# Optimization experiments

Hardware: AMD Instinct MI355X
Metric: run time of the kernel (lower is better)

Reference implementation:

```python
import jax, jax.numpy as jnp
import numpy as np

B, IMG, TXT = 1, 2048, 256
D_MODEL = 2048
HEADS, HEAD_DIM = 16, 128
INNER = HEADS * HEAD_DIM
EPS = 1e-5
SCALE = HEAD_DIM ** -0.5


def _rmsnorm(x, w):
    # normalize over last dim (head_dim)
    return (x * jax.lax.rsqrt(jnp.mean(x * x, axis=-1, keepdims=True) + EPS)) * w


def _rope(x, cos, sin):
    # x: (B, S, H, D); cos/sin: (S, D) with pairwise-repeated freqs (interleaved convention)
    c = cos[None, :, None, :]
    s = sin[None, :, None, :]
    x1 = x[..., 0::2]
    x2 = x[..., 1::2]
    rot = jnp.stack([-x2, x1], axis=-1).reshape(x.shape)
    return x * c + rot * s


def setup_inputs() -> dict:
    key = jax.random.key(0)
    ks = jax.random.split(key, 12)
    sc_in = D_MODEL ** -0.5
    sc_inner = INNER ** -0.5
    inp = {
        'hidden_states': jax.random.normal(ks[0], (B, IMG, D_MODEL), jnp.float32),
        'encoder_hidden_states': jax.random.normal(ks[1], (B, TXT, D_MODEL), jnp.float32),
    }
    # RoPE tables over the joint (text + image) sequence, interleaved pair layout
    pos = jnp.arange(TXT + IMG, dtype=jnp.float32)
    inv = 1.0 / (10000.0 ** (jnp.arange(0, HEAD_DIM, 2, dtype=jnp.float32) / HEAD_DIM))
    freqs = pos[:, None] * inv[None, :]
    freqs = jnp.repeat(freqs, 2, axis=-1)  # (S, HEAD_DIM)
    inp['freqs_cos'] = jnp.cos(freqs)
    inp['freqs_sin'] = jnp.sin(freqs)
    # parameters (stored (in, out))
    inp['Wqkv'] = jax.random.normal(ks[2], (D_MODEL, 3 * INNER), jnp.float32) * sc_in
    inp['Wqkv_add'] = jax.random.normal(ks[3], (D_MODEL, 3 * INNER), jnp.float32) * sc_in
    inp['b_qkv_add'] = jax.random.normal(ks[4], (3 * INNER,), jnp.float32) * 0.01
    inp['norm_q_w'] = jnp.ones((HEAD_DIM,), jnp.float32)
    inp['norm_k_w'] = jnp.ones((HEAD_DIM,), jnp.float32)
    inp['norm_aq_w'] = jnp.ones((HEAD_DIM,), jnp.float32)
    inp['norm_ak_w'] = jnp.ones((HEAD_DIM,), jnp.float32)
    inp['Wout'] = jax.random.normal(ks[5], (INNER, D_MODEL), jnp.float32) * sc_inner
    inp['b_out'] = jax.random.normal(ks[6], (D_MODEL,), jnp.float32) * 0.01
    inp['Wadd_out'] = jax.random.normal(ks[7], (INNER, D_MODEL), jnp.float32) * sc_inner
    inp['b_add_out'] = jax.random.normal(ks[8], (D_MODEL,), jnp.float32) * 0.01
    return inp


def reference(hidden_states, encoder_hidden_states, freqs_cos, freqs_sin,
              Wqkv, Wqkv_add, b_qkv_add, norm_q_w, norm_k_w, norm_aq_w, norm_ak_w,
              Wout, b_out, Wadd_out, b_add_out):
    b, s_img, _ = hidden_states.shape
    s_txt = encoder_hidden_states.shape[1]

    # fused QKV projection (image stream), chunk q/k/v, unflatten heads
    qkv = hidden_states @ Wqkv  # (B, IMG, 3*INNER)
    q, k, v = jnp.split(qkv, 3, axis=-1)
    q = _rmsnorm(q.reshape(b, s_img, HEADS, HEAD_DIM), norm_q_w)
    k = _rmsnorm(k.reshape(b, s_img, HEADS, HEAD_DIM), norm_k_w)
    v = v.reshape(b, s_img, HEADS, HEAD_DIM)

    # fused QKV projection (text stream, with bias)
    eqkv = encoder_hidden_states @ Wqkv_add + b_qkv_add
    eq, ek, ev = jnp.split(eqkv, 3, axis=-1)
    eq = _rmsnorm(eq.reshape(b, s_txt, HEADS, HEAD_DIM), norm_aq_w)
    ek = _rmsnorm(ek.reshape(b, s_txt, HEADS, HEAD_DIM), norm_ak_w)
    ev = ev.reshape(b, s_txt, HEADS, HEAD_DIM)

    # joint [text; image] concatenation, then RoPE on joint Q/K
    jq = jnp.concatenate([eq, q], axis=1)
    jk = jnp.concatenate([ek, k], axis=1)
    jv = jnp.concatenate([ev, v], axis=1)
    jq = _rope(jq, freqs_cos, freqs_sin)
    jk = _rope(jk, freqs_cos, freqs_sin)

    # non-causal scaled dot-product attention, layout (B, S, H, D)
    scores = jnp.einsum('bqhd,bkhd->bhqk', jq, jk) * SCALE
    probs = jax.nn.softmax(scores, axis=-1)
    out = jnp.einsum('bhqk,bkhd->bqhd', probs, jv)  # (B, S_joint, H, D)
    out = out.reshape(b, s_txt + s_img, INNER)

    enc_out = out[:, :s_txt]
    img_out = out[:, s_txt:]
    img_out = img_out @ Wout + b_out
    enc_out = enc_out @ Wadd_out + b_add_out
    return (img_out, enc_out)
```

## Files before the change

### kernel.cpp

```cpp
#include <hip/hip_runtime.h>
#include <stdint.h>

#define HEADS 16
#define HD 128
#define S_TXT 256
#define S_IMG 2048
#define S_ALL 2304
#define DMODEL 2048
#define N_QKV 6144
#define INNER 2048
#define ATT_EPS 1e-5f
#define ATT_SCALE 0.08838834764831845f
#define LOG2E 1.4426950408889634f
#define MBOUND 16.5f
#define QT_N 18
#define TPS 36

typedef __attribute__((ext_vector_type(8))) __bf16 bf16x8;
typedef __attribute__((ext_vector_type(4))) float f32x4;
typedef __attribute__((ext_vector_type(4))) uint32_t u32x4;

__device__ __forceinline__ uint16_t f2bf(float f) {
  union { float f; uint32_t u; } v; v.f = f;
  uint32_t r = (v.u + 0x7FFF + ((v.u >> 16) & 1)) >> 16;
  return (uint16_t)r;
}
__device__ __forceinline__ float bf2f(uint16_t h) {
  union { float f; uint32_t u; } v; v.u = ((uint32_t)h) << 16;
  return v.f;
}
__device__ __forceinline__ float fexp2(float x) {
#if __has_builtin(__builtin_amdgcn_exp2f)
  return __builtin_amdgcn_exp2f(x);
#else
  return __expf(x * 0.69314718055994531f);
#endif
}

__device__ __forceinline__ void async_cp16(const void* g, void* l) {
  __builtin_amdgcn_global_load_lds(
      (const __attribute__((address_space(1))) void*)g,
      (__attribute__((address_space(3))) void*)l, 16, 0, 0);
}

__global__ __launch_bounds__(256) void k_cvt(const float* __restrict__ src,
                                             uint16_t* __restrict__ dst, int n4) {
  int i = blockIdx.x * 256 + threadIdx.x;
  int stride = gridDim.x * 256;
  for (; i < n4; i += stride) {
    float4 v = ((const float4*)src)[i];
    uint16_t o[4];
    o[0] = f2bf(v.x); o[1] = f2bf(v.y); o[2] = f2bf(v.z); o[3] = f2bf(v.w);
    ((uint2*)dst)[i] = *(const uint2*)o;
  }
}

__global__ __launch_bounds__(256) void k_cvt_t4(
    const float* __restrict__ s0, uint16_t* __restrict__ d0,
    const float* __restrict__ s1, uint16_t* __restrict__ d1,
    const float* __restrict__ s2, uint16_t* __restrict__ d2,
    const float* __restrict__ s3, uint16_t* __restrict__ d3) {
  __shared__ float t[64][68];
  int b = blockIdx.x;
  const float* src; uint16_t* dst; int R, C, tb;
  if (b < 3072)      { src = s0; dst = d0; R = DMODEL; C = N_QKV;  tb = b; }
  else if (b < 6144) { src = s1; dst = d1; R = DMODEL; C = N_QKV;  tb = b - 3072; }
  else if (b < 7168) { src = s2; dst = d2; R = INNER;  C = DMODEL; tb = b - 6144; }
  else               { src = s3; dst = d3; R = INNER;  C = DMODEL; tb = b - 7168; }
  int ntr = R >> 6;
  int tr = tb % ntr, tc = tb / ntr;
  int tid = threadIdx.x;
  int rr = tid >> 4, c4 = (tid & 15) * 4;
#pragma unroll
  for (int j = 0; j < 4; ++j) {
    int r = rr + j * 16;
    float4 v = *(const float4*)&src[(size_t)(tr * 64 + r) * C + tc * 64 + c4];
    *(float4*)&t[r][c4] = v;
  }
  __syncthreads();
  int cc = tid >> 4, r4 = (tid & 15) * 4;
#pragma unroll
  for (int j = 0; j < 4; ++j) {
    int c = cc + j * 16;
    uint16_t ov[4];
    ov[0] = f2bf(t[r4 + 0][c]); ov[1] = f2bf(t[r4 + 1][c]);
    ov[2] = f2bf(t[r4 + 2][c]); ov[3] = f2bf(t[r4 + 3][c]);
    *(uint2*)&dst[(size_t)(tc * 64 + c) * R + tr * 64 + r4] = *(const uint2*)ov;
  }
}

__global__ __launch_bounds__(512, 1) void k_gemm2(
    const uint16_t* __restrict__ A0, const uint16_t* __restrict__ B0,
    const float* __restrict__ bias0, uint16_t* __restrict__ C0,
    const uint16_t* __restrict__ A1, const uint16_t* __restrict__ B1,
    const float* __restrict__ bias1, uint16_t* __restrict__ C1,
    int seg0_tiles, int N, int K) {
  __shared__ __align__(16) char lds[3 * 49152];
  int bn = blockIdx.x, bm = blockIdx.y;
  const uint16_t* A; const uint16_t* B; const float* bias; uint16_t* C; int mrow;
  if (bm < seg0_tiles) { A = A0; B = B0; bias = bias0; C = C0; mrow = bm * 256; }
  else { A = A1; B = B1; bias = bias1; C = C1; mrow = (bm - seg0_tiles) * 256; }
  int tid = threadIdx.x, lane = tid & 63, w = tid >> 6;
  int g = lane >> 4, li = lane & 15;
  int wm = w >> 1, wn = w & 1;
  const int NKI = K / 64;

  int rowin = lane >> 3;
  int csrc = (lane & 7) ^ rowin;

  auto stage_a = [&](int t, char* buf, int j0) {
    int kt = t * 64;
#pragma unroll
    for (int j = j0; j < j0 + 2; ++j) {
      int r = w * 4 + j;
      int tr = r * 8 + rowin;
      async_cp16(A + (size_t)(mrow + tr) * K + kt + 8 * csrc, buf + r * 1024);
    }
  };
  auto stage_b = [&](int t, char* buf) {
    int kt = t * 64;
#pragma unroll
    for (int j = 0; j < 2; ++j) {
      int r = w * 2 + j;
      int tr = r * 8 + rowin;
      async_cp16(B + (size_t)(bn * 128 + tr) * K + kt + 8 * csrc, buf + 32768 + r * 1024);
    }
  };

  f32x4 acc[4][4] = {};

  stage_a(0, lds, 0); stage_a(0, lds, 2); stage_b(0, lds);
  stage_a(1, lds + 49152, 0); stage_a(1, lds + 49152, 2); stage_b(1, lds + 49152);
  asm volatile("s_waitcnt vmcnt(6)" ::: "memory");
  __builtin_amdgcn_s_barrier();
  asm volatile("" ::: "memory");

  int cbuf = 0, sbuf = 2;
  for (int t = 0; t < NKI; ++t) {
    const char* cur = lds + cbuf * 49152;
    char* stg = lds + sbuf * 49152;
    bool pre = (t + 2 < NKI);

    bf16x8 af[4], bfv[2];
    if (pre) stage_a(t + 2, stg, 0);
#pragma unroll
    for (int mi = 0; mi < 4; ++mi) {
      int row = wm * 64 + mi * 16 + li;
      af[mi] = __builtin_bit_cast(bf16x8, *(const u32x4*)(cur + row * 128 + (g ^ (row & 7)) * 16));
    }
#pragma unroll
    for (int ni = 0; ni < 2; ++ni) {
      int row = wn * 64 + ni * 16 + li;
      bfv[ni] = __builtin_bit_cast(bf16x8, *(const u32x4*)(cur + 32768 + row * 128 + (g ^ (row & 7)) * 16));
    }
    __builtin_amdgcn_s_barrier();
    __builtin_amdgcn_s_setprio(1);
#pragma unroll
    for (int mi = 0; mi < 4; ++mi)
#pragma unroll
      for (int ni = 0; ni < 2; ++ni)
        acc[mi][ni] = __builtin_amdgcn_mfma_f32_16x16x32_bf16(af[mi], bfv[ni], acc[mi][ni], 0, 0, 0);
    __builtin_amdgcn_s_setprio(0);
    __builtin_amdgcn_s_barrier();

    if (pre) stage_a(t + 2, stg, 2);
#pragma unroll
    for (int ni = 0; ni < 2; ++ni) {
      int row = wn * 64 + (ni + 2) * 16 + li;
      bfv[ni] = __builtin_bit_cast(bf16x8, *(const u32x4*)(cur + 32768 + row * 128 + (g ^ (row & 7)) * 16));
    }
    __builtin_amdgcn_s_barrier();
    __builtin_amdgcn_s_setprio(1);
#pragma unroll
    for (int mi = 0; mi < 4; ++mi)
#pragma unroll
      for (int ni = 0; ni < 2; ++ni)
        acc[mi][ni + 2] = __builtin_amdgcn_mfma_f32_16x16x32_bf16(af[mi], bfv[ni], acc[mi][ni + 2], 0, 0, 0);
    __builtin_amdgcn_s_setprio(0);
    __builtin_amdgcn_s_barrier();

    if (pre) stage_b(t + 2, stg);
#pragma unroll
    for (int mi = 0; mi < 4; ++mi) {
      int row = wm * 64 + mi * 16 + li;
      af[mi] = __builtin_bit_cast(bf16x8, *(const u32x4*)(cur + row * 128 + ((4 + g) ^ (row & 7)) * 16));
    }
#pragma unroll
    for (int ni = 0; ni < 2; ++ni) {
      int row = wn * 64 + ni * 16 + li;
      bfv[ni] = __builtin_bit_cast(bf16x8, *(const u32x4*)(cur + 32768 + row * 128 + ((4 + g) ^ (row & 7)) * 16));
    }
    __builtin_amdgcn_s_barrier();
    __builtin_amdgcn_s_setprio(1);
#pragma unroll
    for (int mi = 0; mi < 4; ++mi)
#pragma unroll
      for (int ni = 0; ni < 2; ++ni)
        acc[mi][ni] = __builtin_amdgcn_mfma_f32_16x16x32_bf16(af[mi], bfv[ni], acc[mi][ni], 0, 0, 0);
    __builtin_amdgcn_s_setprio(0);
    __builtin_amdgcn_s_barrier();

#pragma unroll
    for (int ni = 0; ni < 2; ++ni) {
      int row = wn * 64 + (ni + 2) * 16 + li;
      bfv[ni] = __builtin_bit_cast(bf16x8, *(const u32x4*)(cur + 32768 + row * 128 + ((4 + g) ^ (row & 7)) * 16));
    }
    __builtin_amdgcn_s_barrier();
    __builtin_amdgcn_s_setprio(1);
#pragma unroll
    for (int mi = 0; mi < 4; ++mi)
#pragma unroll
      for (int ni = 0; ni < 2; ++ni)
        acc[mi][ni + 2] = __builtin_amdgcn_mfma_f32_16x16x32_bf16(af[mi], bfv[ni], acc[mi][ni + 2], 0, 0, 0);
    __builtin_amdgcn_s_setprio(0);

    if (t + 1 < NKI) {
      if (pre) asm volatile("s_waitcnt vmcnt(6)" ::: "memory");
      else     asm volatile("s_waitcnt vmcnt(0)" ::: "memory");
    }
    __builtin_amdgcn_s_barrier();
    asm volatile("" ::: "memory");
    cbuf = (cbuf + 1 == 3) ? 0 : cbuf + 1;
    sbuf = (sbuf + 1 == 3) ? 0 : sbuf + 1;
  }

#pragma unroll
  for (int mi = 0; mi < 4; ++mi) {
#pragma unroll
    for (int ni = 0; ni < 4; ++ni) {
      int col = bn * 128 + wn * 64 + ni * 16 + li;
      float bv = bias ? bias[col] : 0.0f;
#pragma unroll
      for (int i = 0; i < 4; ++i) {
        int r = mrow + wm * 64 + mi * 16 + 4 * g + i;
        C[(size_t)r * N + col] = f2bf(acc[mi][ni][i] + bv);
      }
    }
  }
}

__global__ __launch_bounds__(256, 4) void k_gemmO(
    const uint16_t* __restrict__ A0, const uint16_t* __restrict__ B0,
    const float* __restrict__ bias0, float* __restrict__ C0,
    const uint16_t* __restrict__ A1, const uint16_t* __restrict__ B1,
    const float* __restrict__ bias1, float* __restrict__ C1,
    int seg0_tiles, int N, int K) {
  __shared__ __align__(16) char lds[4 * 8192];
  int bn = blockIdx.x, bm = blockIdx.y;
  const uint16_t* A; const uint16_t* B; const float* bias; float* C; int mrow;
  if (bm < seg0_tiles) { A = A0; B = B0; bias = bias0; C = C0; mrow = bm * 128; }
  else { A = A1; B = B1; bias = bias1; C = C1; mrow = (bm - seg0_tiles) * 128; }
  int tid = threadIdx.x, lane = tid & 63, w = tid >> 6;
  int g = lane >> 4, li = lane & 15;
  int wm = w >> 1, wn = w & 1;
  const int NKT = K / 32;

  int rowin = lane >> 2;
  int csrc = (lane & 3) ^ (rowin & 3);

  auto stage = [&](int t, int buf) {
    int kt = t * 32;
#pragma unroll
    for (int j = 0; j < 2; ++j) {
      int r = w * 2 + j;
      int tr = r * 16 + rowin;
      async_cp16(A + (size_t)(mrow + tr) * K + kt + 8 * csrc, lds + buf * 8192 + r * 1024);
    }
#pragma unroll
    for (int j = 0; j < 2; ++j) {
      int r = w * 2 + j;
      int tr = r * 16 + rowin;
      async_cp16(B + (size_t)(bn * 128 + tr) * K + kt + 8 * csrc, lds + 16384 + buf * 8192 + r * 1024);
    }
  };

  f32x4 acc[4][4] = {};
  stage(0, 0);
  asm volatile("s_waitcnt vmcnt(0)" ::: "memory");
  __builtin_amdgcn_s_barrier();
  asm volatile("" ::: "memory");

  for (int t = 0; t < NKT; ++t) {
    int cur = t & 1;
    bool pre = (t + 1 < NKT);
    if (pre) stage(t + 1, cur ^ 1);
    const char* Ac = lds + cur * 8192;
    const char* Bc = lds + 16384 + cur * 8192;

    bf16x8 af[4], bfv[4];
#pragma unroll
    for (int mi = 0; mi < 4; ++mi) {
      int row = wm * 64 + mi * 16 + li;
      af[mi] = __builtin_bit_cast(bf16x8, *(const u32x4*)(Ac + row * 64 + (g ^ (row & 3)) * 16));
    }
#pragma unroll
    for (int ni = 0; ni < 4; ++ni) {
      int row = wn * 64 + ni * 16 + li;
      bfv[ni] = __builtin_bit_cast(bf16x8, *(const u32x4*)(Bc + row * 64 + (g ^ (row & 3)) * 16));
    }
    __builtin_amdgcn_s_setprio(1);
#pragma unroll
    for (int mi = 0; mi < 4; ++mi)
#pragma unroll
      for (int ni = 0; ni < 4; ++ni)
        acc[mi][ni] = __builtin_amdgcn_mfma_f32_16x16x32_bf16(af[mi], bfv[ni], acc[mi][ni], 0, 0, 0);
    __builtin_amdgcn_s_setprio(0);

    if (pre) asm volatile("s_waitcnt vmcnt(0)" ::: "memory");
    __builtin_amdgcn_s_barrier();
    asm volatile("" ::: "memory");
  }

#pragma unroll
  for (int mi = 0; mi < 4; ++mi) {
#pragma unroll
    for (int ni = 0; ni < 4; ++ni) {
      int col = bn * 128 + wn * 64 + ni * 16 + li;
      float bv = bias[col];
#pragma unroll
      for (int i = 0; i < 4; ++i) {
        int r = mrow + wm * 64 + mi * 16 + 4 * g + i;
        C[(size_t)r * N + col] = acc[mi][ni][i] + bv;
      }
    }
  }
}

__global__ __launch_bounds__(256) void k_post(
    const uint16_t* __restrict__ qkv_img, const uint16_t* __restrict__ qkv_txt,
    const float* __restrict__ fcos, const float* __restrict__ fsin,
    const float* __restrict__ wq, const float* __restrict__ wk,
    const float* __restrict__ waq, const float* __restrict__ wak,
    uint16_t* __restrict__ Qo, uint16_t* __restrict__ Ko, uint16_t* __restrict__ VTo) {
  int s = blockIdx.x;
  const uint16_t* row = (s < S_TXT) ? qkv_txt + (size_t)s * N_QKV
                                    : qkv_img + (size_t)(s - S_TXT) * N_QKV;
  const float* wqp = (s < S_TXT) ? waq : wq;
  const float* wkp = (s < S_TXT) ? wak : wk;
  int tid = threadIdx.x, lane = tid & 63, w = tid >> 6;
  int h = w * 4 + (lane >> 4);
  int d0 = (lane & 15) * 8;
  float cs[8], sn[8];
#pragma unroll
  for (int j = 0; j < 8; ++j) {
    cs[j] = fcos[s * HD + d0 + j];
    sn[j] = fsin[s * HD + d0 + j];
  }
#pragma unroll
  for (int part = 0; part < 2; ++part) {
    const uint16_t* src = row + part * INNER + h * HD + d0;
    u32x4 raw = *(const u32x4*)src;
    const uint16_t* rp = (const uint16_t*)&raw;
    float x[8], ss = 0.f;
#pragma unroll
    for (int j = 0; j < 8; ++j) { x[j] = bf2f(rp[j]); ss += x[j] * x[j]; }
    ss += __shfl_xor(ss, 1); ss += __shfl_xor(ss, 2);
    ss += __shfl_xor(ss, 4); ss += __shfl_xor(ss, 8);
    float rn = rsqrtf(ss * (1.0f / HD) + ATT_EPS);
    const float* wp = part ? wkp : wqp;
#pragma unroll
    for (int j = 0; j < 8; ++j) x[j] = x[j] * rn * wp[d0 + j];
    float y[8];
#pragma unroll
    for (int j = 0; j < 8; j += 2) {
      y[j]     = x[j] * cs[j] - x[j + 1] * sn[j];
      y[j + 1] = x[j + 1] * cs[j + 1] + x[j] * sn[j + 1];
    }
    float sc = part ? 1.0f : (ATT_SCALE * LOG2E);
    uint16_t ov[8];
#pragma unroll
    for (int j = 0; j < 8; ++j) ov[j] = f2bf(y[j] * sc);
    uint16_t* dst = (part ? Ko : Qo) + ((size_t)h * S_ALL + s) * HD + d0;
    *(u32x4*)dst = *(const u32x4*)ov;
  }
  {
    u32x4 raw = *(const u32x4*)(row + 2 * INNER + h * HD + d0);
    const uint16_t* rp = (const uint16_t*)&raw;
#pragma unroll
    for (int j = 0; j < 8; ++j)
      VTo[((size_t)h * HD + d0 + j) * S_ALL + s] = rp[j];
  }
}

__global__ __launch_bounds__(256, 3) void k_attn(
    const uint16_t* __restrict__ Qg, const uint16_t* __restrict__ Kg,
    const uint16_t* __restrict__ VTg,
    float* __restrict__ part0, float* __restrict__ part1,
    float* __restrict__ lsumP) {
  __shared__ __align__(16) char Kt[2][8192];
  __shared__ __align__(16) char Vt[2][8192];
  __shared__ __align__(16) uint16_t Pl[4][32 * 40];

  int b0 = blockIdx.x;
  int bid = (b0 & 7) * 72 + (b0 >> 3);
  int h = bid / 36, r6 = bid % 36, sp = r6 / 18, qt = r6 % 18;
  int tid = threadIdx.x, lane = tid & 63, w = tid >> 6;
  int g = lane >> 4, li = lane & 15;

  const uint16_t* Kh = Kg + (size_t)h * S_ALL * HD;
  const uint16_t* Vh = VTg + (size_t)h * HD * S_ALL;
  float* po = (sp ? part1 : part0) + ((size_t)(h * QT_N + qt) * 128 + w * 32) * 128;

  int qbase = qt * 128 + w * 32;
  bf16x8 qf[2][4];
#pragma unroll
  for (int q2 = 0; q2 < 2; ++q2) {
    const uint16_t* qp = Qg + ((size_t)h * S_ALL + qbase + q2 * 16 + li) * HD;
#pragma unroll
    for (int kc = 0; kc < 4; ++kc)
      qf[q2][kc] = __builtin_bit_cast(bf16x8, *(const u32x4*)(qp + kc * 32 + g * 8));
  }
  f32x4 o[2][8] = {};
  float lsum[2] = {0.f, 0.f};

  auto stage = [&](int tk, int buf) {
#pragma unroll
    for (int j = 0; j < 2; ++j) {
      int cj = w * 128 + j * 64 + lane;
      int row = cj >> 4, c = (cj & 15) ^ (row & 15);
      async_cp16(Kh + (size_t)(tk * 32 + row) * HD + 8 * c, Kt[buf] + (w * 128 + j * 64) * 16);
    }
#pragma unroll
    for (int j = 0; j < 2; ++j) {
      int cj = w * 128 + j * 64 + lane;
      int row = cj >> 2, c = (cj & 3) ^ ((row >> 1) & 3);
      async_cp16(Vh + (size_t)row * S_ALL + tk * 32 + 8 * c, Vt[buf] + (w * 128 + j * 64) * 16);
    }
  };

  int t0 = sp * TPS;
  stage(t0, 0);
  asm volatile("s_waitcnt vmcnt(0)" ::: "memory");
  __builtin_amdgcn_s_barrier();
  asm volatile("" ::: "memory");

  for (int t = 0; t < TPS; ++t) {
    int cur = t & 1;
    if (t + 1 < TPS) stage(t0 + t + 1, cur ^ 1);
    const char* KtC = Kt[cur];
    const char* VtC = Vt[cur];

    f32x4 sc[2][2];
#pragma unroll
    for (int q2 = 0; q2 < 2; ++q2)
#pragma unroll
      for (int kb = 0; kb < 2; ++kb)
        sc[q2][kb] = (f32x4){-MBOUND, -MBOUND, -MBOUND, -MBOUND};
    __builtin_amdgcn_s_setprio(1);
#pragma unroll
    for (int kb = 0; kb < 2; ++kb)
#pragma unroll
      for (int kc = 0; kc < 4; ++kc) {
        int ch = (kc * 4 + g) ^ li;
        bf16x8 kf = __builtin_bit_cast(bf16x8,
            *(const u32x4*)(KtC + (kb * 16 + li) * 256 + ch * 16));
        sc[0][kb] = __builtin_amdgcn_mfma_f32_16x16x32_bf16(kf, qf[0][kc], sc[0][kb], 0, 0, 0);
        sc[1][kb] = __builtin_amdgcn_mfma_f32_16x16x32_bf16(kf, qf[1][kc], sc[1][kb], 0, 0, 0);
      }
    __builtin_amdgcn_s_setprio(0);

    uint16_t* Pw = &Pl[w][0];
#pragma unroll
    for (int q2 = 0; q2 < 2; ++q2)
#pragma unroll
      for (int kb = 0; kb < 2; ++kb) {
        float p0 = fexp2(sc[q2][kb][0]);
        float p1 = fexp2(sc[q2][kb][1]);
        float p2 = fexp2(sc[q2][kb][2]);
        float p3 = fexp2(sc[q2][kb][3]);
        lsum[q2] += (p0 + p1) + (p2 + p3);
        uint2 pk;
        pk.x = (uint32_t)f2bf(p0) | ((uint32_t)f2bf(p1) << 16);
        pk.y = (uint32_t)f2bf(p2) | ((uint32_t)f2bf(p3) << 16);
        *(uint2*)((char*)Pw + (q2 * 16 + li) * 80 + kb * 32 + g * 8) = pk;
      }

    bf16x8 pf[2];
#pragma unroll
    for (int q2 = 0; q2 < 2; ++q2)
      pf[q2] = __builtin_bit_cast(bf16x8,
          *(const u32x4*)((const char*)Pw + (q2 * 16 + li) * 80 + g * 16));
    __builtin_amdgcn_s_setprio(1);
#pragma unroll
    for (int db = 0; db < 8; ++db) {
      int vrow = db * 16 + li;
      int ch = g ^ ((vrow >> 1) & 3);
      bf16x8 vf = __builtin_bit_cast(bf16x8, *(const u32x4*)(VtC + vrow * 64 + ch * 16));
      o[0][db] = __builtin_amdgcn_mfma_f32_16x16x32_bf16(pf[0], vf, o[0][db], 0, 0, 0);
      o[1][db] = __builtin_amdgcn_mfma_f32_16x16x32_bf16(pf[1], vf, o[1][db], 0, 0, 0);
    }
    __builtin_amdgcn_s_setprio(0);

    asm volatile("s_waitcnt vmcnt(0)" ::: "memory");
    __builtin_amdgcn_s_barrier();
    asm volatile("" ::: "memory");
  }

#pragma unroll
  for (int q2 = 0; q2 < 2; ++q2) {
    float v = lsum[q2];
    v += __shfl_xor(v, 16);
    v += __shfl_xor(v, 32);
    lsum[q2] = v;
  }
  if (lane < 16) {
#pragma unroll
    for (int q2 = 0; q2 < 2; ++q2)
      lsumP[((size_t)sp * HEADS + h) * S_ALL + qbase + q2 * 16 + lane] = lsum[q2];
  }
#pragma unroll
  for (int q2 = 0; q2 < 2; ++q2)
#pragma unroll
    for (int db = 0; db < 8; ++db)
#pragma unroll
      for (int i = 0; i < 4; ++i)
        po[(q2 * 16 + 4 * g + i) * 128 + db * 16 + li] = o[q2][db][i];
}

__global__ __launch_bounds__(256) void k_comb(
    const float* __restrict__ p0, const float* __restrict__ p1,
    const float* __restrict__ lsumP, uint16_t* __restrict__ attn) {
  int q = blockIdx.x, qt = q >> 7, ql = q & 127;
#pragma unroll
  for (int rep = 0; rep < 2; ++rep) {
    int d4 = threadIdx.x + rep * 256;
    int d = d4 * 4, h = d >> 7, dl = d & 127;
    size_t off = (((size_t)h * QT_N + qt) * 128 + ql) * 128 + dl;
    float4 a = *(const float4*)&p0[off];
    float4 b = *(const float4*)&p1[off];
    float l0 = lsumP[(size_t)h * S_ALL + q];
    float l1 = lsumP[((size_t)HEADS + h) * S_ALL + q];
    float inv = 1.0f / (l0 + l1);
    uint16_t ov[4];
    ov[0] = f2bf((a.x + b.x) * inv); ov[1] = f2bf((a.y + b.y) * inv);
    ov[2] = f2bf((a.z + b.z) * inv); ov[3] = f2bf((a.w + b.w) * inv);
    *(uint2*)&attn[(size_t)q * INNER + d] = *(const uint2*)ov;
  }
}

extern "C" void kernel_launch(void* const* d_in, const int* in_sizes, int n_in,
                              void* d_out, int out_size, void* d_ws, size_t ws_size,
                              hipStream_t stream) {
  const float* hidden = (const float*)d_in[0];
  const float* enc    = (const float*)d_in[1];
  const float* fcos   = (const float*)d_in[2];
  const float* fsin   = (const float*)d_in[3];
  const float* Wqkv   = (const float*)d_in[4];
  const float* Wqkva  = (const float*)d_in[5];
  const float* bqkva  = (const float*)d_in[6];
  const float* nqw    = (const float*)d_in[7];
  const float* nkw    = (const float*)d_in[8];
  const float* naqw   = (const float*)d_in[9];
  const float* nakw   = (const float*)d_in[10];
  const float* Wout   = (const float*)d_in[11];
  const float* bout   = (const float*)d_in[12];
  const float* Wadd   = (const float*)d_in[13];
  const float* badd   = (const float*)d_in[14];
  float* out_img = (float*)d_out;
  float* out_enc = (float*)d_out + (size_t)S_IMG * DMODEL;

  char* ws = (char*)d_ws;
  size_t off = 0;
  auto alloc = [&](size_t bytes) {
    char* p = ws + off;
    off += (bytes + 255) & ~(size_t)255;
    return p;
  };
  uint16_t* hs_bf   = (uint16_t*)alloc((size_t)S_IMG * DMODEL * 2);
  uint16_t* enc_bf  = (uint16_t*)alloc((size_t)S_TXT * DMODEL * 2);
  char*     wqkv_base = alloc((size_t)N_QKV * DMODEL * 2 * 2);
  uint16_t* WqkvT   = (uint16_t*)wqkv_base;
  uint16_t* WqkvaT  = (uint16_t*)(wqkv_base + (size_t)N_QKV * DMODEL * 2);
  uint16_t* WoutT   = (uint16_t*)alloc((size_t)DMODEL * INNER * 2);
  uint16_t* WaddT   = (uint16_t*)alloc((size_t)DMODEL * INNER * 2);
  uint16_t* qkv_img = (uint16_t*)alloc((size_t)S_IMG * N_QKV * 2);
  uint16_t* qkv_txt = (uint16_t*)alloc((size_t)S_TXT * N_QKV * 2);
  uint16_t* Qb   = (uint16_t*)wqkv_base;
  uint16_t* Kb   = Qb + (size_t)HEADS * S_ALL * HD;
  uint16_t* VTb  = Kb + (size_t)HEADS * S_ALL * HD;
  uint16_t* attn = VTb + (size_t)HEADS * S_ALL * HD;
  float* part0 = (float*)d_out;
  float* part1 = (float*)qkv_img;
  float* lsumP = (float*)enc_bf;

  k_cvt<<<1024, 256, 0, stream>>>(hidden, hs_bf, S_IMG * DMODEL / 4);
  k_cvt<<<256, 256, 0, stream>>>(enc, enc_bf, S_TXT * DMODEL / 4);
  k_cvt_t4<<<8192, 256, 0, stream>>>(Wqkv, WqkvT, Wqkva, WqkvaT, Wout, WoutT, Wadd, WaddT);

  dim3 gq(N_QKV / 128, (S_TXT + S_IMG) / 256);
  k_gemm2<<<gq, 512, 0, stream>>>(enc_bf, WqkvaT, bqkva, qkv_txt,
                                  hs_bf, WqkvT, nullptr, qkv_img,
                                  1, N_QKV, DMODEL);

  k_post<<<S_ALL, 256, 0, stream>>>(qkv_img, qkv_txt, fcos, fsin,
                                    nqw, nkw, naqw, nakw, Qb, Kb, VTb);

  k_attn<<<HEADS * QT_N * 2, 256, 0, stream>>>(Qb, Kb, VTb, part0, part1, lsumP);
  k_comb<<<S_ALL, 256, 0, stream>>>(part0, part1, lsumP, attn);

  dim3 go(DMODEL / 128, S_ALL / 128);
  k_gemmO<<<go, 256, 0, stream>>>(attn, WaddT, badd, out_enc,
                                  attn + (size_t)S_TXT * INNER, WoutT, bout, out_img,
                                  2, DMODEL, DMODEL);
}
```

Measured before the change: 258.8 us.

## Coalesce V transpose via LDS kernel, simplify QKV GEMM inner loop

V transpose moves out of k_post into a new k_vt kernel that stages 64x128 tiles in LDS and writes 16-byte coalesced rows, replacing scattered 2-byte stores. The QKV GEMM main loop drops its four-phase interleaved load/MFMA schedule with barriers in favour of one stage call, loading all fragments for both k-halves and issuing 32 MFMAs per step. The weight transpose tile padding changes from 68 to 65. The transpose rework adds a kernel launch, and the GEMM change raises register pressure and loses the fine-grained overlap between loads and MFMAs.

After: 235.6 us. 1.1x faster.

```diff
diff --git a/kernel.cpp b/kernel.cpp
--- a/kernel.cpp
+++ b/kernel.cpp
@@ -60,7 +60,7 @@
     const float* __restrict__ s1, uint16_t* __restrict__ d1,
     const float* __restrict__ s2, uint16_t* __restrict__ d2,
     const float* __restrict__ s3, uint16_t* __restrict__ d3) {
-  __shared__ float t[64][68];
+  __shared__ float t[64][65];
   int b = blockIdx.x;
   const float* src; uint16_t* dst; int R, C, tb;
   if (b < 3072)      { src = s0; dst = d0; R = DMODEL; C = N_QKV;  tb = b; }
@@ -108,17 +108,14 @@
   int rowin = lane >> 3;
   int csrc = (lane & 7) ^ rowin;
 
-  auto stage_a = [&](int t, char* buf, int j0) {
+  auto stage = [&](int t, char* buf) {
     int kt = t * 64;
 #pragma unroll
-    for (int j = j0; j < j0 + 2; ++j) {
+    for (int j = 0; j < 4; ++j) {
       int r = w * 4 + j;
       int tr = r * 8 + rowin;
       async_cp16(A + (size_t)(mrow + tr) * K + kt + 8 * csrc, buf + r * 1024);
     }
-  };
-  auto stage_b = [&](int t, char* buf) {
-    int kt = t * 64;
 #pragma unroll
     for (int j = 0; j < 2; ++j) {
       int r = w * 2 + j;
@@ -129,8 +126,8 @@
 
   f32x4 acc[4][4] = {};
 
-  stage_a(0, lds, 0); stage_a(0, lds, 2); stage_b(0, lds);
-  stage_a(1, lds + 49152, 0); stage_a(1, lds + 49152, 2); stage_b(1, lds + 49152);
+  stage(0, lds);
+  stage(1, lds + 49152);
   asm volatile("s_waitcnt vmcnt(6)" ::: "memory");
   __builtin_amdgcn_s_barrier();
   asm volatile("" ::: "memory");
@@ -138,88 +135,40 @@
   int cbuf = 0, sbuf = 2;
   for (int t = 0; t < NKI; ++t) {
     const char* cur = lds + cbuf * 49152;
-    char* stg = lds + sbuf * 49152;
-    bool pre = (t + 2 < NKI);
-
-    bf16x8 af[4], bfv[2];
-    if (pre) stage_a(t + 2, stg, 0);
-#pragma unroll
-    for (int mi = 0; mi < 4; ++mi) {
-      int row = wm * 64 + mi * 16 + li;
-      af[mi] = __builtin_bit_cast(bf16x8, *(const u32x4*)(cur + row * 128 + (g ^ (row & 7)) * 16));
-    }
-#pragma unroll
-    for (int ni = 0; ni < 2; ++ni) {
-      int row = wn * 64 + ni * 16 + li;
-      bfv[ni] = __builtin_bit_cast(bf16x8, *(const u32x4*)(cur + 32768 + row * 128 + (g ^ (row & 7)) * 16));
-    }
-    __builtin_amdgcn_s_barrier();
+    if (t + 2 < NKI) stage(t + 2, lds + sbuf * 49152);
+
+    bf16x8 af[2][4], bfv[2][4];
+#pragma unroll
+    for (int kk = 0; kk < 2; ++kk) {
+#pragma unroll
+      for (int mi = 0; mi < 4; ++mi) {
+        int row = wm * 64 + mi * 16 + li;
+        int ch = (kk * 4 + g) ^ (row & 7);
+        af[kk][mi] = __builtin_bit_cast(bf16x8, *(const u32x4*)(cur + row * 128 + ch * 16));
+      }
+#pragma unroll
+      for (int ni = 0; ni < 4; ++ni) {
+        int row = wn * 64 + ni * 16 + li;
+        int ch = (kk * 4 + g) ^ (row & 7);
+        bfv[kk][ni] = __builtin_bit_cast(bf16x8, *(const u32x4*)(cur + 32768 + row * 128 + ch * 16));
+      }
+    }
     __builtin_amdgcn_s_setprio(1);
 #pragma unroll
-    for (int mi = 0; mi < 4; ++mi)
-#pragma unroll
-      for (int ni = 0; ni < 2; ++ni)
-        acc[mi][ni] = __builtin_amdgcn_mfma_f32_16x16x32_bf16(af[mi], bfv[ni], acc[mi][ni], 0, 0, 0);
+    for (int kk = 0; kk < 2; ++kk)
+#pragma unroll
+      for (int mi = 0; mi < 4; ++mi)
+#pragma unroll
+        for (int ni = 0; ni < 4; ++ni)
+          acc[mi][ni] = __builtin_amdgcn_mfma_f32_16x16x32_bf16(af[kk][mi], bfv[kk][ni], acc[mi][ni], 0, 0, 0);
     __builtin_amdgcn_s_setprio(0);
-    __builtin_amdgcn_s_barrier();
-
-    if (pre) stage_a(t + 2, stg, 2);
-#pragma unroll
-    for (int ni = 0; ni < 2; ++ni) {
-      int row = wn * 64 + (ni + 2) * 16 + li;
-      bfv[ni] = __builtin_bit_cast(bf16x8, *(const u32x4*)(cur + 32768 + row * 128 + (g ^ (row & 7)) * 16));
-    }
-    __builtin_amdgcn_s_barrier();
-    __builtin_amdgcn_s_setprio(1);
-#pragma unroll
-    for (int mi = 0; mi < 4; ++mi)
-#pragma unroll
-      for (int ni = 0; ni < 2; ++ni)
-        acc[mi][ni + 2] = __builtin_amdgcn_mfma_f32_16x16x32_bf16(af[mi], bfv[ni], acc[mi][ni + 2], 0, 0, 0);
-    __builtin_amdgcn_s_setprio(0);
-    __builtin_amdgcn_s_barrier();
-
-    if (pre) stage_b(t + 2, stg);
-#pragma unroll
-    for (int mi = 0; mi < 4; ++mi) {
-      int row = wm * 64 + mi * 16 + li;
-      af[mi] = __builtin_bit_cast(bf16x8, *(const u32x4*)(cur + row * 128 + ((4 + g) ^ (row & 7)) * 16));
-    }
-#pragma unroll
-    for (int ni = 0; ni < 2; ++ni) {
-      int row = wn * 64 + ni * 16 + li;
-      bfv[ni] = __builtin_bit_cast(bf16x8, *(const u32x4*)(cur + 32768 + row * 128 + ((4 + g) ^ (row & 7)) * 16));
-    }
-    __builtin_amdgcn_s_barrier();
-    __builtin_amdgcn_s_setprio(1);
-#pragma unroll
-    for (int mi = 0; mi < 4; ++mi)
-#pragma unroll
-      for (int ni = 0; ni < 2; ++ni)
-        acc[mi][ni] = __builtin_amdgcn_mfma_f32_16x16x32_bf16(af[mi], bfv[ni], acc[mi][ni], 0, 0, 0);
-    __builtin_amdgcn_s_setprio(0);
-    __builtin_amdgcn_s_barrier();
-
-#pragma unroll
-    for (int ni = 0; ni < 2; ++ni) {
-      int row = wn * 64 + (ni + 2) * 16 + li;
-      bfv[ni] = __builtin_bit_cast(bf16x8, *(const u32x4*)(cur + 32768 + row * 128 + ((4 + g) ^ (row & 7)) * 16));
-    }
-    __builtin_amdgcn_s_barrier();
-    __builtin_amdgcn_s_setprio(1);
-#pragma unroll
-    for (int mi = 0; mi < 4; ++mi)
-#pragma unroll
-      for (int ni = 0; ni < 2; ++ni)
-        acc[mi][ni + 2] = __builtin_amdgcn_mfma_f32_16x16x32_bf16(af[mi], bfv[ni], acc[mi][ni + 2], 0, 0, 0);
-    __builtin_amdgcn_s_setprio(0);
 
     if (t + 1 < NKI) {
-      if (pre) asm volatile("s_waitcnt vmcnt(6)" ::: "memory");
-      else     asm volatile("s_waitcnt vmcnt(0)" ::: "memory");
-    }
-    __builtin_amdgcn_s_barrier();
-    asm volatile("" ::: "memory");
+      if (t + 2 < NKI) asm volatile("s_waitcnt vmcnt(6)" ::: "memory");
+      else             asm volatile("s_waitcnt vmcnt(0)" ::: "memory");
+      __builtin_amdgcn_s_barrier();
+      asm volatile("" ::: "memory");
+    }
     cbuf = (cbuf + 1 == 3) ? 0 : cbuf + 1;
     sbuf = (sbuf + 1 == 3) ? 0 : sbuf + 1;
   }
@@ -331,7 +280,7 @@
     const float* __restrict__ fcos, const float* __restrict__ fsin,
     const float* __restrict__ wq, const float* __restrict__ wk,
     const float* __restrict__ waq, const float* __restrict__ wak,
-    uint16_t* __restrict__ Qo, uint16_t* __restrict__ Ko, uint16_t* __restrict__ VTo) {
+    uint16_t* __restrict__ Qo, uint16_t* __restrict__ Ko) {
   int s = blockIdx.x;
   const uint16_t* row = (s < S_TXT) ? qkv_txt + (size_t)s * N_QKV
                                     : qkv_img + (size_t)(s - S_TXT) * N_QKV;
@@ -373,12 +322,33 @@
     uint16_t* dst = (part ? Ko : Qo) + ((size_t)h * S_ALL + s) * HD + d0;
     *(u32x4*)dst = *(const u32x4*)ov;
   }
-  {
-    u32x4 raw = *(const u32x4*)(row + 2 * INNER + h * HD + d0);
-    const uint16_t* rp = (const uint16_t*)&raw;
-#pragma unroll
-    for (int j = 0; j < 8; ++j)
-      VTo[((size_t)h * HD + d0 + j) * S_ALL + s] = rp[j];
+}
+
+__global__ __launch_bounds__(256) void k_vt(
+    const uint16_t* __restrict__ qkv_img, const uint16_t* __restrict__ qkv_txt,
+    uint16_t* __restrict__ VTo) {
+  __shared__ uint16_t Vl[64][136];
+  int st = blockIdx.x % 36, h = blockIdx.x / 36;
+  int s0 = st * 64;
+  const uint16_t* base = (s0 < S_TXT) ? qkv_txt + (size_t)s0 * N_QKV
+                                      : qkv_img + (size_t)(s0 - S_TXT) * N_QKV;
+  base += 2 * INNER + h * HD;
+  int tid = threadIdx.x;
+#pragma unroll
+  for (int it = 0; it < 4; ++it) {
+    int idx = it * 256 + tid;
+    int r = idx >> 4, c = idx & 15;
+    *(u32x4*)&Vl[r][c * 8] = *(const u32x4*)(base + (size_t)r * N_QKV + c * 8);
+  }
+  __syncthreads();
+#pragma unroll
+  for (int it = 0; it < 4; ++it) {
+    int idx = it * 256 + tid;
+    int d = idx >> 3, sc = (idx & 7) * 8;
+    uint16_t tmp[8];
+#pragma unroll
+    for (int j = 0; j < 8; ++j) tmp[j] = Vl[sc + j][d];
+    *(u32x4*)&VTo[((size_t)h * HD + d) * S_ALL + s0 + sc] = *(const u32x4*)tmp;
   }
 }
 
@@ -593,7 +563,8 @@
                                   1, N_QKV, DMODEL);
 
   k_post<<<S_ALL, 256, 0, stream>>>(qkv_img, qkv_txt, fcos, fsin,
-                                    nqw, nkw, naqw, nakw, Qb, Kb, VTb);
+                                    nqw, nkw, naqw, nakw, Qb, Kb);
+  k_vt<<<36 * HEADS, 256, 0, stream>>>(qkv_img, qkv_txt, VTb);
 
   k_attn<<<HEADS * QT_N * 2, 256, 0, stream>>>(Qb, Kb, VTb, part0, part1, lsumP);
   k_comb<<<S_ALL, 256, 0, stream>>>(part0, part1, lsumP, attn);
```
